# Optimization experiments

Measured on AMD Instinct MI355X. Metric: run time of the kernel, lower is better.

The kernel has to match this reference:

```python
import jax, jax.numpy as jnp
import numpy as np

U, I, NB = 200000, 100000, 50000
D = 64
NUM_LAYERS = 2
TEMP = 0.25      # conf['c_temps']
ALPHA = 0.5      # conf['alpha']
E_UI, E_UB, E_BI = 4_000_000, 2_000_000, 2_000_000
BT = 4096


def _segsum(vals, idx, gathered, n):
    # SpMM: out[idx] += vals * gathered   (COO sparse matmul)
    return jax.ops.segment_sum(vals[:, None] * gathered, idx, num_segments=n)


def _propagate(xa, xb, rows, cols, vals, layers):
    # LightGCN-style propagation over the symmetric bipartite block matrix
    # [[0, A], [A^T, 0]] with layer averaging.
    acc_a, acc_b = xa, xb
    for _ in range(layers):
        na = _segsum(vals, rows, xb[cols], xa.shape[0])
        nb = _segsum(vals, cols, xa[rows], xb.shape[0])
        xa, xb = na, nb
        acc_a = acc_a + xa
        acc_b = acc_b + xb
    inv = 1.0 / (layers + 1)
    return acc_a * inv, acc_b * inv


def _info_nce(a, b, temp):
    a = a * jax.lax.rsqrt(jnp.sum(a * a, -1, keepdims=True) + 1e-8)
    b = b * jax.lax.rsqrt(jnp.sum(b * b, -1, keepdims=True) + 1e-8)
    logits = (a @ b.T) / temp                      # [BT, BT]
    return jnp.mean(jax.nn.logsumexp(logits, axis=-1) - jnp.diagonal(logits))


def setup_inputs() -> dict:
    key = jax.random.key(0)
    ks = jax.random.split(key, 20)
    sc = 1.0 / np.sqrt(D)
    f32 = jnp.float32
    return {
        "users_feat": jax.random.normal(ks[0], (U, D), f32) * sc,
        "bundles_feat": jax.random.normal(ks[1], (NB, D), f32) * sc,
        "items_feat": jax.random.normal(ks[2], (I, D), f32) * sc,
        "L1_w": jax.random.normal(ks[3], (3, 3), f32) * 0.5,
        "L1_b": jnp.zeros((3,), f32),
        "L2_w": jax.random.normal(ks[4], (3, 3), f32) * 0.5,
        "L2_b": jnp.zeros((3,), f32),
        "L3_w": jax.random.normal(ks[5], (1, 3), f32) * 0.5,
        "L3_b": jnp.zeros((1,), f32),
        "ui_val": jax.random.uniform(ks[6], (E_UI,), f32, 0.0, 0.05),
        "ub_val": jax.random.uniform(ks[7], (E_UB,), f32, 0.0, 0.05),
        "bi_val": jax.random.uniform(ks[8], (E_BI,), f32, 0.0, 0.05),
        "ui_row": jax.random.randint(ks[9], (E_UI,), 0, U, jnp.int32),
        "ui_col": jax.random.randint(ks[10], (E_UI,), 0, I, jnp.int32),
        "ub_row": jax.random.randint(ks[11], (E_UB,), 0, U, jnp.int32),
        "ub_col": jax.random.randint(ks[12], (E_UB,), 0, NB, jnp.int32),
        "bi_row": jax.random.randint(ks[13], (E_BI,), 0, NB, jnp.int32),
        "bi_col": jax.random.randint(ks[14], (E_BI,), 0, I, jnp.int32),
        "users_idx": jax.random.randint(ks[15], (BT,), 0, U, jnp.int32),
        "bundles_idx": jax.random.randint(ks[16], (BT, 2), 0, NB, jnp.int32),
    }


def reference(users_feat, bundles_feat, items_feat, L1_w, L1_b, L2_w, L2_b,
              L3_w, L3_b, ui_val, ub_val, bi_val, ui_row, ui_col, ub_row,
              ub_col, bi_row, bi_col, users_idx, bundles_idx):
    # View 1: item-level main graph (u-i Laplacian propagation), bundle rep
    # aggregated from item embeddings via the row-normalized b-i graph.
    u1, i1 = _propagate(users_feat, items_feat, ui_row, ui_col, ui_val, NUM_LAYERS)
    b1 = _segsum(bi_val, bi_row, i1[bi_col], NB)
    # View 2: bundle-level main graph (u-b Laplacian propagation).
    u2, b2 = _propagate(users_feat, bundles_feat, ub_row, ub_col, ub_val, NUM_LAYERS)
    # View 3: sub views, one-hop row-normalized aggregation of raw item embs.
    u3 = _segsum(ui_val, ui_row, items_feat[ui_col], U)
    b3 = _segsum(bi_val, bi_row, items_feat[bi_col], NB)

    ue = jnp.stack([u1[users_idx], u2[users_idx], u3[users_idx]], axis=-1)      # [BT,D,3]
    be = jnp.stack([b1[bundles_idx], b2[bundles_idx], b3[bundles_idx]], axis=-1)  # [BT,2,D,3]
    s = jnp.einsum('bdv,bpdv->bpv', ue, be)                                      # [BT,2,3]

    # L1/L2/L3 view-fusion MLP (3 -> 3 -> 3 -> 1)
    h = jnp.tanh(s @ L1_w.T + L1_b)
    h = jnp.tanh(h @ L2_w.T + L2_b)
    pred = (h @ L3_w.T + L3_b)[..., 0]                                           # [BT,2]

    # BPR: -log sigmoid(pos - neg) == softplus(neg - pos)
    bpr = jnp.mean(jax.nn.softplus(-(pred[:, 0] - pred[:, 1])))
    cl = (_info_nce(u1[users_idx], u2[users_idx], TEMP)
          + _info_nce(b1[bundles_idx[:, 0]], b2[bundles_idx[:, 0]], TEMP))
    return bpr + ALPHA * cl
```

## Files before the change

kernel.cpp:

```cpp
#include <hip/hip_runtime.h>
#include <math.h>

#define DD 64
#define SCAN_TPB 256
#define SCAN_EPT 8
#define SCAN_EPB (SCAN_TPB * SCAN_EPT)
#define NCHUNK 8

typedef short bf16x8 __attribute__((ext_vector_type(8)));
typedef float f32x4 __attribute__((ext_vector_type(4)));

__device__ __forceinline__ float bf2f(unsigned short u) {
    return __uint_as_float(((unsigned)u) << 16);
}
__device__ __forceinline__ unsigned short f2bf(float x) {
    unsigned b = __float_as_uint(x);
    unsigned r = (b + 0x7fffu + ((b >> 16) & 1u)) >> 16;
    return (unsigned short)r;
}


__global__ void hist_chunked_kernel(int* __restrict__ cnt, const int* __restrict__ tgt,
                                    int E, int n) {
    int myc = blockIdx.x & (NCHUNK - 1);
    int sub = blockIdx.x >> 3;
    int nsub = gridDim.x >> 3;
    int start = sub * blockDim.x + threadIdx.x;
    int stride = nsub * blockDim.x;
    for (int e = start; e < E; e += stride) {
        int t_ = tgt[e];
        int c = (int)(((long long)t_ * NCHUNK) / n);
        if (c == myc) atomicAdd(&cnt[t_], 1);
    }
}

__global__ void scatter_pairs_chunked(int2* __restrict__ pairs, int* __restrict__ cursor,
                                      const int* __restrict__ tgt, const int* __restrict__ src,
                                      const float* __restrict__ val, int E, int n) {
    int myc = blockIdx.x & (NCHUNK - 1);
    int sub = blockIdx.x >> 3;
    int nsub = gridDim.x >> 3;
    int start = sub * blockDim.x + threadIdx.x;
    int stride = nsub * blockDim.x;
    for (int e = start; e < E; e += stride) {
        int t_ = tgt[e];
        int c = (int)(((long long)t_ * NCHUNK) / n);
        if (c == myc) {
            int2 pr;
            pr.x = src[e];
            pr.y = __float_as_int(val[e]);
            int p = atomicAdd(&cursor[t_], 1);
            pairs[p] = pr;
        }
    }
}

__global__ void mark_kernel(int* __restrict__ mark, const int* __restrict__ idx, int n) {
    int g = blockIdx.x * blockDim.x + threadIdx.x;
    if (g < n) mark[idx[g]] = 1;
}

__global__ void hist_marked_kernel(int* __restrict__ cnt, const int* __restrict__ tgt,
                                   const int* __restrict__ mark, int E) {
    int g = blockIdx.x * blockDim.x + threadIdx.x;
    int stride = gridDim.x * blockDim.x;
    for (int e = g; e < E; e += stride) {
        int t_ = tgt[e];
        if (mark[t_]) atomicAdd(&cnt[t_], 1);
    }
}

__global__ void scatter_marked_kernel(int2* __restrict__ pairs, int* __restrict__ cursor,
                                      const int* __restrict__ tgt, const int* __restrict__ src,
                                      const float* __restrict__ val,
                                      const int* __restrict__ mark, int E) {
    int g = blockIdx.x * blockDim.x + threadIdx.x;
    int stride = gridDim.x * blockDim.x;
    for (int e = g; e < E; e += stride) {
        int t_ = tgt[e];
        if (mark[t_]) {
            int2 pr;
            pr.x = src[e];
            pr.y = __float_as_int(val[e]);
            int p = atomicAdd(&cursor[t_], 1);
            pairs[p] = pr;
        }
    }
}

__global__ void scan_pass1(int* __restrict__ blocksum, const int* __restrict__ cnt, int n) {
    int base = blockIdx.x * SCAN_EPB + threadIdx.x * SCAN_EPT;
    int s = 0;
#pragma unroll
    for (int k = 0; k < SCAN_EPT; ++k) {
        int i = base + k;
        if (i < n) s += cnt[i];
    }
#pragma unroll
    for (int o = 32; o >= 1; o >>= 1) s += __shfl_xor(s, o);
    __shared__ int ws_[4];
    if ((threadIdx.x & 63) == 0) ws_[threadIdx.x >> 6] = s;
    __syncthreads();
    if (threadIdx.x == 0) blocksum[blockIdx.x] = ws_[0] + ws_[1] + ws_[2] + ws_[3];
}

__global__ void scan_pass2(int* __restrict__ blocksum, int nb, int* __restrict__ ptr_n) {
    __shared__ int sh[1024];
    int t = threadIdx.x;
    int v = (t < nb) ? blocksum[t] : 0;
    sh[t] = v;
    __syncthreads();
    for (int o = 1; o < 1024; o <<= 1) {
        int x = (t >= o) ? sh[t - o] : 0;
        __syncthreads();
        sh[t] += x;
        __syncthreads();
    }
    if (t < nb) blocksum[t] = sh[t] - v;
    if (t == nb - 1) ptr_n[0] = sh[t];
}

__global__ void scan_pass3(int* __restrict__ ptr, int* __restrict__ cursor,
                           const int* __restrict__ cnt, const int* __restrict__ blockoff,
                           int n) {
    int base = blockIdx.x * SCAN_EPB + threadIdx.x * SCAN_EPT;
    int vals[SCAN_EPT];
    int s = 0;
#pragma unroll
    for (int k = 0; k < SCAN_EPT; ++k) {
        int i = base + k;
        int c = (i < n) ? cnt[i] : 0;
        vals[k] = s;
        s += c;
    }
    int incl = s;
#pragma unroll
    for (int o = 1; o < 64; o <<= 1) {
        int x = __shfl_up(incl, o);
        if ((threadIdx.x & 63) >= o) incl += x;
    }
    __shared__ int wtot[4];
    if ((threadIdx.x & 63) == 63) wtot[threadIdx.x >> 6] = incl;
    __syncthreads();
    int woff = 0;
    int wv = threadIdx.x >> 6;
    for (int k = 0; k < 4; ++k)
        if (k < wv) woff += wtot[k];
    int texcl = incl - s + woff + blockoff[blockIdx.x];
#pragma unroll
    for (int k = 0; k < SCAN_EPT; ++k) {
        int i = base + k;
        if (i < n) {
            int p = texcl + vals[k];
            ptr[i] = p;
            cursor[i] = p;
        }
    }
}

__global__ void spmm2_kernel(const unsigned short* __restrict__ inb,
                             const int2* __restrict__ pairs, const int* __restrict__ ptr,
                             int nrows,
                             float* __restrict__ out, unsigned short* __restrict__ outb) {
    int wp = (int)(((unsigned)blockIdx.x * blockDim.x + threadIdx.x) >> 6);
    int lane = threadIdx.x & 63;
    int w0 = wp * 2;
    if (w0 >= nrows) return;
    bool two = (w0 + 1 < nrows);
    int pA = ptr[w0];
    int endA = ptr[w0 + 1];
    int pB = two ? endA : 0;
    int endB = two ? ptr[w0 + 2] : 0;
    float accA = 0.f, accB = 0.f;
    while (endA - pA >= 8 && endB - pB >= 8) {
        int sA[8], sB[8];
        float vA[8], vB[8];
#pragma unroll
        for (int k = 0; k < 8; ++k) {
            int2 a = pairs[pA + k];
            int2 b = pairs[pB + k];
            sA[k] = __builtin_amdgcn_readfirstlane(a.x);
            vA[k] = __int_as_float(__builtin_amdgcn_readfirstlane(a.y));
            sB[k] = __builtin_amdgcn_readfirstlane(b.x);
            vB[k] = __int_as_float(__builtin_amdgcn_readfirstlane(b.y));
        }
#pragma unroll
        for (int k = 0; k < 8; ++k) {
            accA += vA[k] * bf2f(inb[(size_t)sA[k] * DD + lane]);
            accB += vB[k] * bf2f(inb[(size_t)sB[k] * DD + lane]);
        }
        pA += 8;
        pB += 8;
    }
    for (; pA + 8 <= endA; pA += 8) {
        int ss[8];
        float vv[8];
#pragma unroll
        for (int k = 0; k < 8; ++k) {
            int2 pr = pairs[pA + k];
            ss[k] = __builtin_amdgcn_readfirstlane(pr.x);
            vv[k] = __int_as_float(__builtin_amdgcn_readfirstlane(pr.y));
        }
#pragma unroll
        for (int k = 0; k < 8; ++k) accA += vv[k] * bf2f(inb[(size_t)ss[k] * DD + lane]);
    }
    for (; pA < endA; ++pA) {
        int2 pr = pairs[pA];
        int s = __builtin_amdgcn_readfirstlane(pr.x);
        float v = __int_as_float(__builtin_amdgcn_readfirstlane(pr.y));
        accA += v * bf2f(inb[(size_t)s * DD + lane]);
    }
    for (; pB + 8 <= endB; pB += 8) {
        int ss[8];
        float vv[8];
#pragma unroll
        for (int k = 0; k < 8; ++k) {
            int2 pr = pairs[pB + k];
            ss[k] = __builtin_amdgcn_readfirstlane(pr.x);
            vv[k] = __int_as_float(__builtin_amdgcn_readfirstlane(pr.y));
        }
#pragma unroll
        for (int k = 0; k < 8; ++k) accB += vv[k] * bf2f(inb[(size_t)ss[k] * DD + lane]);
    }
    for (; pB < endB; ++pB) {
        int2 pr = pairs[pB];
        int s = __builtin_amdgcn_readfirstlane(pr.x);
        float v = __int_as_float(__builtin_amdgcn_readfirstlane(pr.y));
        accB += v * bf2f(inb[(size_t)s * DD + lane]);
    }
    size_t offA = (size_t)w0 * DD + lane;
    if (out) {
        out[offA] = accA;
        if (two) out[offA + DD] = accB;
    }
    if (outb) {
        outb[offA] = f2bf(accA);
        if (two) outb[offA + DD] = f2bf(accB);
    }
}

__global__ void spmm_kernel(const float* __restrict__ inf, const unsigned short* __restrict__ inb,
                            const int2* __restrict__ pairs, const int* __restrict__ ptr,
                            int nrows, const int* __restrict__ rowidx,
                            float* __restrict__ out, unsigned short* __restrict__ outb,
                            const float* __restrict__ add1,
                            const float* __restrict__ add2f,
                            const unsigned short* __restrict__ add2b,
                            float scale1,
                            const float* __restrict__ in2f, const unsigned short* __restrict__ in2b,
                            float* __restrict__ out2, const float* __restrict__ addB,
                            float f, float scale2,
                            unsigned short* __restrict__ nrmOut, int nrmEvery) {
    int w = (int)(((unsigned)blockIdx.x * blockDim.x + threadIdx.x) >> 6);
    int lane = threadIdx.x & 63;
    if (w >= nrows) return;
    int r = rowidx ? rowidx[w] : w;
    int p = ptr[r];
    int end = ptr[r + 1];
    size_t outoff = (size_t)w * DD + lane;
    size_t nodeoff = (size_t)r * DD + lane;
    float acc = 0.f, acc2 = 0.f;
    const bool dual = (in2f != nullptr) || (in2b != nullptr);
    for (; p + 8 <= end; p += 8) {
        int ss[8];
        float vv[8];
#pragma unroll
        for (int k = 0; k < 8; ++k) {
            int2 pr = pairs[p + k];
            ss[k] = __builtin_amdgcn_readfirstlane(pr.x);
            vv[k] = __int_as_float(__builtin_amdgcn_readfirstlane(pr.y));
        }
        if (inb) {
#pragma unroll
            for (int k = 0; k < 8; ++k) acc += vv[k] * bf2f(inb[(size_t)ss[k] * DD + lane]);
        } else {
#pragma unroll
            for (int k = 0; k < 8; ++k) acc += vv[k] * inf[(size_t)ss[k] * DD + lane];
        }
        if (dual) {
            if (in2b) {
#pragma unroll
                for (int k = 0; k < 8; ++k) acc2 += vv[k] * bf2f(in2b[(size_t)ss[k] * DD + lane]);
            } else {
#pragma unroll
                for (int k = 0; k < 8; ++k) acc2 += vv[k] * in2f[(size_t)ss[k] * DD + lane];
            }
        }
    }
    for (; p < end; ++p) {
        int2 pr = pairs[p];
        int s = __builtin_amdgcn_readfirstlane(pr.x);
        float v = __int_as_float(__builtin_amdgcn_readfirstlane(pr.y));
        acc += v * (inb ? bf2f(inb[(size_t)s * DD + lane]) : inf[(size_t)s * DD + lane]);
        if (dual)
            acc2 += v * (in2b ? bf2f(in2b[(size_t)s * DD + lane]) : in2f[(size_t)s * DD + lane]);
    }
    float rr = acc;
    if (add1) rr += add1[nodeoff];
    if (add2f) rr += add2f[nodeoff];
    if (add2b) rr += bf2f(add2b[nodeoff]);
    rr *= scale1;
    if (out) out[outoff] = rr;
    if (outb) outb[outoff] = f2bf(rr);
    if (dual) {
        float r2 = acc2 + f * acc;
        if (addB) r2 += addB[nodeoff];
        out2[outoff] = r2 * scale2;
    }
    if (nrmOut && (nrmEvery == 1 || (w & 1) == 0)) {
        float sq = rr * rr;
#pragma unroll
        for (int o = 32; o >= 1; o >>= 1) sq += __shfl_xor(sq, o);
        nrmOut[(size_t)(w / nrmEvery) * DD + lane] = f2bf(rr * rsqrtf(sq + 1e-8f));
    }
}


__global__ void f2bf_kernel(unsigned short* __restrict__ o, const float* __restrict__ i,
                            long long n4) {
    long long g = (long long)blockIdx.x * blockDim.x + threadIdx.x;
    long long stride = (long long)gridDim.x * blockDim.x;
    for (long long t = g; t < n4; t += stride) {
        float4 v = ((const float4*)i)[t];
        ushort4 u;
        u.x = f2bf(v.x); u.y = f2bf(v.y); u.z = f2bf(v.z); u.w = f2bf(v.w);
        ((ushort4*)o)[t] = u;
    }
}

__global__ void gather_rows_bf16_kernel(float* __restrict__ raw,
                                        const unsigned short* __restrict__ src,
                                        const int* __restrict__ idx, int nrows) {
    int g = blockIdx.x * blockDim.x + threadIdx.x;
    if (g >= nrows * DD) return;
    int r = g >> 6;
    raw[g] = bf2f(src[(size_t)idx[r] * DD + (g & 63)]);
}

__global__ void batch_pred_kernel(const float* __restrict__ u1b, const float* __restrict__ u2b,
                                  const float* __restrict__ u3b,
                                  const float* __restrict__ b1b, const float* __restrict__ b2b,
                                  const float* __restrict__ b3b,
                                  const float* __restrict__ W1, const float* __restrict__ c1,
                                  const float* __restrict__ W2, const float* __restrict__ c2,
                                  const float* __restrict__ W3, const float* __restrict__ c3,
                                  float* __restrict__ acc, int nb) {
    int b = blockIdx.x;
    if (b >= nb) return;
    int d = threadIdx.x;
    float ud1 = u1b[(size_t)b * DD + d];
    float ud2 = u2b[(size_t)b * DD + d];
    float ud3 = u3b[(size_t)b * DD + d];
    float pred[2];
#pragma unroll
    for (int p = 0; p < 2; ++p) {
        size_t r = (size_t)(b * 2 + p) * DD + d;
        float s0 = ud1 * b1b[r];
        float s1 = ud2 * b2b[r];
        float s2 = ud3 * b3b[r];
#pragma unroll
        for (int o = 32; o >= 1; o >>= 1) {
            s0 += __shfl_xor(s0, o);
            s1 += __shfl_xor(s1, o);
            s2 += __shfl_xor(s2, o);
        }
        float t0 = tanhf(s0 * W1[0] + s1 * W1[1] + s2 * W1[2] + c1[0]);
        float t1 = tanhf(s0 * W1[3] + s1 * W1[4] + s2 * W1[5] + c1[1]);
        float t2 = tanhf(s0 * W1[6] + s1 * W1[7] + s2 * W1[8] + c1[2]);
        float g0 = tanhf(t0 * W2[0] + t1 * W2[1] + t2 * W2[2] + c2[0]);
        float g1 = tanhf(t0 * W2[3] + t1 * W2[4] + t2 * W2[5] + c2[1]);
        float g2 = tanhf(t0 * W2[6] + t1 * W2[7] + t2 * W2[8] + c2[2]);
        pred[p] = g0 * W3[0] + g1 * W3[1] + g2 * W3[2] + c3[0];
    }
    if (d == 0) {
        float x = pred[1] - pred[0];
        float sp = (x > 20.0f) ? x : log1pf(expf(x));
        unsafeAtomicAdd(acc, sp);
    }
}

__global__ void nce_mfma_kernel(const unsigned short* __restrict__ A1,
                                const unsigned short* __restrict__ B1, float* __restrict__ acc1,
                                const unsigned short* __restrict__ A2,
                                const unsigned short* __restrict__ B2, float* __restrict__ acc2,
                                int n, float invtemp) {
    int nbv = n >> 4;
    const unsigned short* A;
    const unsigned short* B;
    float* accp;
    int blk = blockIdx.x;
    if (blk < nbv) { A = A1; B = B1; accp = acc1; }
    else           { blk -= nbv; A = A2; B = B2; accp = acc2; }
    int row0 = blk << 4;
    int wv = threadIdx.x >> 6, lane = threadIdx.x & 63;
    int li = lane & 15, lq = lane >> 4;

    const bf16x8* Ap = (const bf16x8*)(A + (size_t)(row0 + li) * DD + lq * 8);
    bf16x8 af0 = Ap[0];
    bf16x8 af1 = Ap[4];

    int qcols = n >> 2;
    int c0 = wv * qcols;
    int ntile = qcols >> 4;
    float m[4] = {-1e30f, -1e30f, -1e30f, -1e30f};
    float sm[4] = {0.f, 0.f, 0.f, 0.f};
    float dg[4] = {0.f, 0.f, 0.f, 0.f};
    for (int t = 0; t < ntile; ++t) {
        int colbase = c0 + (t << 4);
        const bf16x8* Bp = (const bf16x8*)(B + (size_t)(colbase + li) * DD + lq * 8);
        bf16x8 bf0 = Bp[0];
        bf16x8 bf1 = Bp[4];
        f32x4 z = {0.f, 0.f, 0.f, 0.f};
        f32x4 s = __builtin_amdgcn_mfma_f32_16x16x32_bf16(af0, bf0, z, 0, 0, 0);
        s = __builtin_amdgcn_mfma_f32_16x16x32_bf16(af1, bf1, s, 0, 0, 0);
        int col = colbase + li;
#pragma unroll
        for (int r = 0; r < 4; ++r) {
            float l = s[r] * invtemp;
            int row = row0 + (lq << 2) + r;
            if (col == row) dg[r] = l;
            float mn = fmaxf(m[r], l);
            sm[r] = sm[r] * __expf(m[r] - mn) + __expf(l - mn);
            m[r] = mn;
        }
    }
#pragma unroll
    for (int r = 0; r < 4; ++r) {
        float mm = m[r], ss = sm[r], dd = dg[r];
#pragma unroll
        for (int o = 1; o <= 8; o <<= 1) {
            float m2 = __shfl_xor(mm, o);
            float s2 = __shfl_xor(ss, o);
            float d2 = __shfl_xor(dd, o);
            float mn = fmaxf(mm, m2);
            ss = ss * __expf(mm - mn) + s2 * __expf(m2 - mn);
            mm = mn;
            dd += d2;
        }
        m[r] = mm; sm[r] = ss; dg[r] = dd;
    }
    __shared__ float pM[4][16], pS[4][16], pD[4][16];
    if (li == 0) {
#pragma unroll
        for (int r = 0; r < 4; ++r) {
            pM[wv][(lq << 2) + r] = m[r];
            pS[wv][(lq << 2) + r] = sm[r];
            pD[wv][(lq << 2) + r] = dg[r];
        }
    }
    __syncthreads();
    if (wv == 0 && lane < 16) {
        float mm = -1e30f, ss = 0.f, dd = 0.f;
#pragma unroll
        for (int q = 0; q < 4; ++q) {
            float mq = pM[q][lane], sq = pS[q][lane];
            dd += pD[q][lane];
            float mn = fmaxf(mm, mq);
            ss = ss * __expf(mm - mn) + sq * __expf(mq - mn);
            mm = mn;
        }
        float v = mm + logf(ss) - dd;
#pragma unroll
        for (int o = 1; o <= 8; o <<= 1) v += __shfl_xor(v, o);
        if (lane == 0) unsafeAtomicAdd(accp, v);
    }
}

__global__ void final_kernel(const float* __restrict__ acc, float* __restrict__ out,
                             float invn, float alpha) {
    out[0] = acc[0] * invn + alpha * invn * (acc[1] + acc[2]);
}


extern "C" void kernel_launch(void* const* d_in, const int* in_sizes, int n_in,
                              void* d_out, int out_size, void* d_ws, size_t ws_size,
                              hipStream_t stream) {
    const float* users_feat   = (const float*)d_in[0];
    const float* bundles_feat = (const float*)d_in[1];
    const float* items_feat   = (const float*)d_in[2];
    const float* W1 = (const float*)d_in[3];
    const float* c1 = (const float*)d_in[4];
    const float* W2 = (const float*)d_in[5];
    const float* c2 = (const float*)d_in[6];
    const float* W3 = (const float*)d_in[7];
    const float* c3 = (const float*)d_in[8];
    const float* ui_val = (const float*)d_in[9];
    const float* ub_val = (const float*)d_in[10];
    const float* bi_val = (const float*)d_in[11];
    const int* ui_row = (const int*)d_in[12];
    const int* ui_col = (const int*)d_in[13];
    const int* ub_row = (const int*)d_in[14];
    const int* ub_col = (const int*)d_in[15];
    const int* bi_row = (const int*)d_in[16];
    const int* bi_col = (const int*)d_in[17];
    const int* uidx = (const int*)d_in[18];
    const int* bidx = (const int*)d_in[19];

    const int U  = in_sizes[0] / DD;
    const int NB = in_sizes[1] / DD;
    const int I  = in_sizes[2] / DD;
    const int Eui = in_sizes[9];
    const int Eub = in_sizes[10];
    const int Ebi = in_sizes[11];
    const int BT = in_sizes[18];

    const size_t U64  = (size_t)U * DD;
    const size_t I64  = (size_t)I * DD;
    const size_t NB64 = (size_t)NB * DD;
    const size_t BT64 = (size_t)BT * DD;

    float* w = (float*)d_ws;
    size_t o = 0;
    float* RA  = w + o; o += I64;
    float* RB  = w + o; o += I64;
    float* u3b = w + o; o += BT64;
    float* u1b = w + o; o += BT64;
    float* u2b = w + o; o += BT64;
    float* b1b = w + o; o += 2 * BT64;
    float* b2b = w + o; o += 2 * BT64;
    float* b3b = w + o; o += 2 * BT64;
    unsigned short* A1  = (unsigned short*)(w + o); o += BT64 / 2;
    unsigned short* A2  = (unsigned short*)(w + o); o += BT64 / 2;
    unsigned short* B1n = (unsigned short*)(w + o); o += BT64 / 2;
    unsigned short* B2n = (unsigned short*)(w + o); o += BT64 / 2;
    float* acc = w + o; o += 16;

    unsigned short* Ubf = (unsigned short*)(w + o); o += (U64 + 1) / 2;
    unsigned short* Ibf = (unsigned short*)(w + o); o += (I64 + 1) / 2;
    unsigned short* Bbf = (unsigned short*)(w + o); o += (NB64 + 1) / 2;
    unsigned short* Xbf = (unsigned short*)(w + o); o += (U64 + 1) / 2;

    int nmax = U; if (I > nmax) nmax = I; if (NB > nmax) nmax = NB;
    int emax = Eui; if (Eub > emax) emax = Eub; if (Ebi > emax) emax = Ebi;
    int* ib = (int*)(w + o);
    size_t io_ = 0;
    int* cnt  = ib + io_; io_ += (size_t)nmax + 1;
    int* bsum = ib + io_; io_ += 1025;
    int* mark = ib + io_; io_ += (size_t)NB + 1;
    int* ptrA = ib + io_; io_ += (size_t)nmax + 1;
    int* ptrB = ib + io_; io_ += (size_t)nmax + 1;
    io_ = (io_ + 3) & ~(size_t)3;
    int2* pairsA = (int2*)(ib + io_); io_ += (size_t)emax * 2;
    int2* pairsB = (int2*)(ib + io_); io_ += (size_t)emax * 2;

    auto build = [&](int2* pairs, int* ptr_, const int* tgt, const int* src,
                     const float* val, int n, int E) {
        hipMemsetAsync(cnt, 0, ((size_t)n + 1) * sizeof(int), stream);
        hist_chunked_kernel<<<8192, 256, 0, stream>>>(cnt, tgt, E, n);
        int nb_ = (n + SCAN_EPB - 1) / SCAN_EPB;
        scan_pass1<<<nb_, SCAN_TPB, 0, stream>>>(bsum, cnt, n);
        scan_pass2<<<1, 1024, 0, stream>>>(bsum, nb_, ptr_ + n);
        scan_pass3<<<nb_, SCAN_TPB, 0, stream>>>(ptr_, cnt, cnt, bsum, n);
        scatter_pairs_chunked<<<8192, 256, 0, stream>>>(pairs, cnt, tgt, src, val, E, n);
    };
    auto spmm = [&](const float* inf, const unsigned short* inb,
                    const int2* pairs, const int* ptr_, int nrows, const int* rowidx,
                    float* out, unsigned short* outb,
                    const float* add1, const float* add2f, const unsigned short* add2b,
                    float scale1,
                    const float* in2f, const unsigned short* in2b,
                    float* out2, const float* addB, float f, float scale2,
                    unsigned short* nrmOut, int nrmEvery) {
        int blocks = (nrows + 3) / 4;
        spmm_kernel<<<blocks, 256, 0, stream>>>(inf, inb, pairs, ptr_, nrows, rowidx,
                                                out, outb, add1, add2f, add2b, scale1,
                                                in2f, in2b, out2, addB, f, scale2,
                                                nrmOut, nrmEvery);
    };
    auto spmm2 = [&](const unsigned short* inb, const int2* pairs, const int* ptr_,
                     int nrows, float* out, unsigned short* outb) {
        int blocks = (nrows + 7) / 8;
        spmm2_kernel<<<blocks, 256, 0, stream>>>(inb, pairs, ptr_, nrows, out, outb);
    };
    const float k3 = 1.0f / 3.0f;
    const float* NF = nullptr;
    const unsigned short* NB16 = nullptr;

    f2bf_kernel<<<2048, 256, 0, stream>>>(Ubf, users_feat, (long long)(U64 / 4));
    f2bf_kernel<<<1024, 256, 0, stream>>>(Ibf, items_feat, (long long)(I64 / 4));
    f2bf_kernel<<<512, 256, 0, stream>>>(Bbf, bundles_feat, (long long)(NB64 / 4));

    build(pairsA, ptrA, ui_row, ui_col, ui_val, U, Eui);
    spmm2(Ibf, pairsA, ptrA, U, nullptr, Xbf);
    gather_rows_bf16_kernel<<<(BT * DD + 255) / 256, 256, 0, stream>>>(u3b, Xbf, uidx, BT);
    build(pairsB, ptrB, ui_col, ui_row, ui_val, I, Eui);
    spmm(NF, Ubf, pairsB, ptrB, I, nullptr,
         RA, nullptr, NF, NF, NB16, 1.f,
         NF, Xbf, RB, items_feat, 1.f, k3,
         nullptr, 1);
    spmm(RA, NB16, pairsA, ptrA, BT, uidx,
         u1b, nullptr, users_feat, NF, Xbf, k3, NF, NB16, nullptr, NF, 0.f, 1.f,
         A1, 1);
    hipMemsetAsync(mark, 0, ((size_t)NB + 1) * sizeof(int), stream);
    mark_kernel<<<(2 * BT + 255) / 256, 256, 0, stream>>>(mark, bidx, 2 * BT);
    hipMemsetAsync(cnt, 0, ((size_t)NB + 1) * sizeof(int), stream);
    {
        int gb = (Ebi + 255) / 256; if (gb > 4096) gb = 4096;
        hist_marked_kernel<<<gb, 256, 0, stream>>>(cnt, bi_row, mark, Ebi);
        int nb_ = (NB + SCAN_EPB - 1) / SCAN_EPB;
        scan_pass1<<<nb_, SCAN_TPB, 0, stream>>>(bsum, cnt, NB);
        scan_pass2<<<1, 1024, 0, stream>>>(bsum, nb_, ptrA + NB);
        scan_pass3<<<nb_, SCAN_TPB, 0, stream>>>(ptrA, cnt, cnt, bsum, NB);
        scatter_marked_kernel<<<gb, 256, 0, stream>>>(pairsA, cnt, bi_row, bi_col,
                                                      bi_val, mark, Ebi);
    }
    spmm(RB, NB16, pairsA, ptrA, 2 * BT, bidx,
         b1b, nullptr, NF, NF, NB16, 1.f,
         NF, Ibf, b3b, NF, 0.f, 1.f,
         B1n, 2);

    build(pairsA, ptrA, ub_row, ub_col, ub_val, U, Eub);
    spmm2(Bbf, pairsA, ptrA, U, nullptr, Xbf);
    build(pairsB, ptrB, ub_col, ub_row, ub_val, NB, Eub);
    spmm2(Ubf, pairsB, ptrB, NB, RA, nullptr);
    spmm(RA, NB16, pairsA, ptrA, BT, uidx,
         u2b, nullptr, users_feat, NF, Xbf, k3, NF, NB16, nullptr, NF, 0.f, 1.f,
         A2, 1);
    spmm(NF, Xbf, pairsB, ptrB, 2 * BT, bidx,
         b2b, nullptr, bundles_feat, RA, NB16, k3, NF, NB16, nullptr, NF, 0.f, 1.f,
         B2n, 2);

    hipMemsetAsync(acc, 0, 4 * sizeof(float), stream);

    batch_pred_kernel<<<BT, 64, 0, stream>>>(u1b, u2b, u3b, b1b, b2b, b3b,
                                             W1, c1, W2, c2, W3, c3, acc, BT);

    nce_mfma_kernel<<<2 * (BT / 16), 256, 0, stream>>>(A1, A2, acc + 1,
                                                       B1n, B2n, acc + 2, BT, 4.0f);

    final_kernel<<<1, 1, 0, stream>>>(acc, (float*)d_out, 1.0f / (float)BT, 0.5f);
}
```

Baseline: 1.992 ms.

## Build both CSR directions in one pass and merge paired launches

```diff
diff --git a/kernel.cpp b/kernel.cpp
--- a/kernel.cpp
+++ b/kernel.cpp
@@ -18,39 +18,53 @@
     unsigned r = (b + 0x7fffu + ((b >> 16) & 1u)) >> 16;
     return (unsigned short)r;
 }
-
-
-__global__ void hist_chunked_kernel(int* __restrict__ cnt, const int* __restrict__ tgt,
-                                    int E, int n) {
+__device__ __forceinline__ int chunk_of(int t, int n) {
+    return (int)(((long long)t * NCHUNK) / n);
+}
+
+
+__global__ void hist2_chunked(int* __restrict__ cntA, const int* __restrict__ tgtA, int nA,
+                              int* __restrict__ cntB, const int* __restrict__ tgtB, int nB,
+                              int E) {
     int myc = blockIdx.x & (NCHUNK - 1);
     int sub = blockIdx.x >> 3;
     int nsub = gridDim.x >> 3;
     int start = sub * blockDim.x + threadIdx.x;
     int stride = nsub * blockDim.x;
     for (int e = start; e < E; e += stride) {
-        int t_ = tgt[e];
-        int c = (int)(((long long)t_ * NCHUNK) / n);
-        if (c == myc) atomicAdd(&cnt[t_], 1);
-    }
-}
-
-__global__ void scatter_pairs_chunked(int2* __restrict__ pairs, int* __restrict__ cursor,
-                                      const int* __restrict__ tgt, const int* __restrict__ src,
-                                      const float* __restrict__ val, int E, int n) {
+        int a = tgtA[e];
+        if (chunk_of(a, nA) == myc) atomicAdd(&cntA[a], 1);
+        int b = tgtB[e];
+        if (chunk_of(b, nB) == myc) atomicAdd(&cntB[b], 1);
+    }
+}
+
+__global__ void scatter2_chunked(int2* __restrict__ pairsA, int* __restrict__ curA, int nA,
+                                 int2* __restrict__ pairsB, int* __restrict__ curB, int nB,
+                                 const int* __restrict__ rowA, const int* __restrict__ colA,
+                                 const float* __restrict__ val, int E) {
     int myc = blockIdx.x & (NCHUNK - 1);
     int sub = blockIdx.x >> 3;
     int nsub = gridDim.x >> 3;
     int start = sub * blockDim.x + threadIdx.x;
     int stride = nsub * blockDim.x;
     for (int e = start; e < E; e += stride) {
-        int t_ = tgt[e];
-        int c = (int)(((long long)t_ * NCHUNK) / n);
-        if (c == myc) {
-            int2 pr;
-            pr.x = src[e];
-            pr.y = __float_as_int(val[e]);
-            int p = atomicAdd(&cursor[t_], 1);
-            pairs[p] = pr;
+        int r = rowA[e];
+        int ci = colA[e];
+        bool mA = (chunk_of(r, nA) == myc);
+        bool mB = (chunk_of(ci, nB) == myc);
+        if (mA || mB) {
+            int v = __float_as_int(val[e]);
+            if (mA) {
+                int p = atomicAdd(&curA[r], 1);
+                int2 pr; pr.x = ci; pr.y = v;
+                pairsA[p] = pr;
+            }
+            if (mB) {
+                int q = atomicAdd(&curB[ci], 1);
+                int2 pr; pr.x = r; pr.y = v;
+                pairsB[q] = pr;
+            }
         }
     }
 }
@@ -88,8 +102,9 @@
     }
 }
 
-__global__ void scan_pass1(int* __restrict__ blocksum, const int* __restrict__ cnt, int n) {
-    int base = blockIdx.x * SCAN_EPB + threadIdx.x * SCAN_EPT;
+__device__ __forceinline__ void scan_p1_body(int* blocksum, const int* cnt, int n, int lb,
+                                             int t) {
+    int base = lb * SCAN_EPB + t * SCAN_EPT;
     int s = 0;
 #pragma unroll
     for (int k = 0; k < SCAN_EPT; ++k) {
@@ -99,14 +114,13 @@
 #pragma unroll
     for (int o = 32; o >= 1; o >>= 1) s += __shfl_xor(s, o);
     __shared__ int ws_[4];
-    if ((threadIdx.x & 63) == 0) ws_[threadIdx.x >> 6] = s;
+    if ((t & 63) == 0) ws_[t >> 6] = s;
     __syncthreads();
-    if (threadIdx.x == 0) blocksum[blockIdx.x] = ws_[0] + ws_[1] + ws_[2] + ws_[3];
-}
-
-__global__ void scan_pass2(int* __restrict__ blocksum, int nb, int* __restrict__ ptr_n) {
+    if (t == 0) blocksum[lb] = ws_[0] + ws_[1] + ws_[2] + ws_[3];
+}
+
+__device__ __forceinline__ void scan_p2_body(int* blocksum, int nb, int* tot, int t) {
     __shared__ int sh[1024];
-    int t = threadIdx.x;
     int v = (t < nb) ? blocksum[t] : 0;
     sh[t] = v;
     __syncthreads();
@@ -117,13 +131,12 @@
         __syncthreads();
     }
     if (t < nb) blocksum[t] = sh[t] - v;
-    if (t == nb - 1) ptr_n[0] = sh[t];
-}
-
-__global__ void scan_pass3(int* __restrict__ ptr, int* __restrict__ cursor,
-                           const int* __restrict__ cnt, const int* __restrict__ blockoff,
-                           int n) {
-    int base = blockIdx.x * SCAN_EPB + threadIdx.x * SCAN_EPT;
+    if (t == nb - 1) tot[0] = sh[t];
+}
+
+__device__ __forceinline__ void scan_p3_body(int* ptr, int* cursor, const int* cnt,
+                                             const int* blockoff, int n, int lb, int t) {
+    int base = lb * SCAN_EPB + t * SCAN_EPT;
     int vals[SCAN_EPT];
     int s = 0;
 #pragma unroll
@@ -137,16 +150,16 @@
 #pragma unroll
     for (int o = 1; o < 64; o <<= 1) {
         int x = __shfl_up(incl, o);
-        if ((threadIdx.x & 63) >= o) incl += x;
+        if ((t & 63) >= o) incl += x;
     }
     __shared__ int wtot[4];
-    if ((threadIdx.x & 63) == 63) wtot[threadIdx.x >> 6] = incl;
+    if ((t & 63) == 63) wtot[t >> 6] = incl;
     __syncthreads();
     int woff = 0;
-    int wv = threadIdx.x >> 6;
+    int wv = t >> 6;
     for (int k = 0; k < 4; ++k)
         if (k < wv) woff += wtot[k];
-    int texcl = incl - s + woff + blockoff[blockIdx.x];
+    int texcl = incl - s + woff + blockoff[lb];
 #pragma unroll
     for (int k = 0; k < SCAN_EPT; ++k) {
         int i = base + k;
@@ -158,12 +171,46 @@
     }
 }
 
-__global__ void spmm2_kernel(const unsigned short* __restrict__ inb,
-                             const int2* __restrict__ pairs, const int* __restrict__ ptr,
-                             int nrows,
-                             float* __restrict__ out, unsigned short* __restrict__ outb) {
-    int wp = (int)(((unsigned)blockIdx.x * blockDim.x + threadIdx.x) >> 6);
-    int lane = threadIdx.x & 63;
+__global__ void scan_pass1(int* __restrict__ bsum, const int* __restrict__ cnt, int n) {
+    scan_p1_body(bsum, cnt, n, blockIdx.x, threadIdx.x);
+}
+__global__ void scan_pass2(int* __restrict__ bsum, int nb, int* __restrict__ tot) {
+    scan_p2_body(bsum, nb, tot, threadIdx.x);
+}
+__global__ void scan_pass3(int* __restrict__ ptr, int* __restrict__ cursor,
+                           const int* __restrict__ cnt, const int* __restrict__ boff, int n) {
+    scan_p3_body(ptr, cursor, cnt, boff, n, blockIdx.x, threadIdx.x);
+}
+
+__global__ void scan2_pass1(int* __restrict__ bsumA, const int* __restrict__ cntA, int nA,
+                            int nbA,
+                            int* __restrict__ bsumB, const int* __restrict__ cntB, int nB) {
+    int b = blockIdx.x;
+    if (b < nbA) scan_p1_body(bsumA, cntA, nA, b, threadIdx.x);
+    else         scan_p1_body(bsumB, cntB, nB, b - nbA, threadIdx.x);
+}
+__global__ void scan2_pass2(int* __restrict__ bsumA, int nbA, int* __restrict__ totA,
+                            int* __restrict__ bsumB, int nbB, int* __restrict__ totB) {
+    if (blockIdx.x == 0) scan_p2_body(bsumA, nbA, totA, threadIdx.x);
+    else                 scan_p2_body(bsumB, nbB, totB, threadIdx.x);
+}
+__global__ void scan2_pass3(int* __restrict__ ptrA, int* __restrict__ curA,
+                            const int* __restrict__ cntA, const int* __restrict__ boffA,
+                            int nA, int nbA,
+                            int* __restrict__ ptrB, int* __restrict__ curB,
+                            const int* __restrict__ cntB, const int* __restrict__ boffB,
+                            int nB) {
+    int b = blockIdx.x;
+    if (b < nbA) scan_p3_body(ptrA, curA, cntA, boffA, nA, b, threadIdx.x);
+    else         scan_p3_body(ptrB, curB, cntB, boffB, nB, b - nbA, threadIdx.x);
+}
+
+__device__ __forceinline__ void spmm2_rows(const unsigned short* __restrict__ inb,
+                                           const int2* __restrict__ pairs,
+                                           const int* __restrict__ ptr, int nrows,
+                                           float* __restrict__ out,
+                                           unsigned short* __restrict__ outb,
+                                           int wp, int lane) {
     int w0 = wp * 2;
     if (w0 >= nrows) return;
     bool two = (w0 + 1 < nrows);
@@ -207,8 +254,8 @@
     for (; pA < endA; ++pA) {
         int2 pr = pairs[pA];
         int s = __builtin_amdgcn_readfirstlane(pr.x);
-        float v = __int_as_float(__builtin_amdgcn_readfirstlane(pr.y));
-        accA += v * bf2f(inb[(size_t)s * DD + lane]);
+        accA += __int_as_float(__builtin_amdgcn_readfirstlane(pr.y)) *
+                bf2f(inb[(size_t)s * DD + lane]);
     }
     for (; pB + 8 <= endB; pB += 8) {
         int ss[8];
@@ -225,8 +272,8 @@
     for (; pB < endB; ++pB) {
         int2 pr = pairs[pB];
         int s = __builtin_amdgcn_readfirstlane(pr.x);
-        float v = __int_as_float(__builtin_amdgcn_readfirstlane(pr.y));
-        accB += v * bf2f(inb[(size_t)s * DD + lane]);
+        accB += __int_as_float(__builtin_amdgcn_readfirstlane(pr.y)) *
+                bf2f(inb[(size_t)s * DD + lane]);
     }
     size_t offA = (size_t)w0 * DD + lane;
     if (out) {
@@ -236,6 +283,32 @@
     if (outb) {
         outb[offA] = f2bf(accA);
         if (two) outb[offA + DD] = f2bf(accB);
+    }
+}
+
+__global__ void spmm2_kernel(const unsigned short* __restrict__ inb,
+                             const int2* __restrict__ pairs, const int* __restrict__ ptr,
+                             int nrows, float* __restrict__ out,
+                             unsigned short* __restrict__ outb) {
+    int wp = (int)(((unsigned)blockIdx.x * blockDim.x + threadIdx.x) >> 6);
+    spmm2_rows(inb, pairs, ptr, nrows, out, outb, wp, threadIdx.x & 63);
+}
+
+__global__ void spmm2_dual_kernel(const unsigned short* __restrict__ inbA,
+                                  const int2* __restrict__ pairsA, const int* __restrict__ ptrA,
+                                  int nrowsA, unsigned short* __restrict__ outbA,
+                                  const unsigned short* __restrict__ inbB,
+                                  const int2* __restrict__ pairsB, const int* __restrict__ ptrB,
+                                  int nrowsB, float* __restrict__ outB) {
+    int nblkA = (nrowsA + 7) / 8;
+    int blk = blockIdx.x;
+    int lane = threadIdx.x & 63;
+    int wvb = threadIdx.x >> 6;
+    if (blk < nblkA) {
+        spmm2_rows(inbA, pairsA, ptrA, nrowsA, nullptr, outbA, blk * 4 + wvb, lane);
+    } else {
+        blk -= nblkA;
+        spmm2_rows(inbB, pairsB, ptrB, nrowsB, outB, nullptr, blk * 4 + wvb, lane);
     }
 }
 
@@ -316,15 +389,26 @@
 }
 
 
-__global__ void f2bf_kernel(unsigned short* __restrict__ o, const float* __restrict__ i,
-                            long long n4) {
+__global__ void f2bf3_kernel(unsigned short* __restrict__ o1, const float* __restrict__ i1,
+                             long long n1,
+                             unsigned short* __restrict__ o2, const float* __restrict__ i2,
+                             long long n2,
+                             unsigned short* __restrict__ o3, const float* __restrict__ i3,
+                             long long n3) {
     long long g = (long long)blockIdx.x * blockDim.x + threadIdx.x;
     long long stride = (long long)gridDim.x * blockDim.x;
-    for (long long t = g; t < n4; t += stride) {
-        float4 v = ((const float4*)i)[t];
+    long long tot = n1 + n2 + n3;
+    for (long long t = g; t < tot; t += stride) {
+        const float* ip;
+        unsigned short* op;
+        long long j = t;
+        if (j < n1) { ip = i1; op = o1; }
+        else if (j < n1 + n2) { j -= n1; ip = i2; op = o2; }
+        else { j -= n1 + n2; ip = i3; op = o3; }
+        float4 v = ((const float4*)ip)[j];
         ushort4 u;
         u.x = f2bf(v.x); u.y = f2bf(v.y); u.z = f2bf(v.z); u.w = f2bf(v.w);
-        ((ushort4*)o)[t] = u;
+        ((ushort4*)op)[j] = u;
     }
 }
 
@@ -534,24 +618,31 @@
     int emax = Eui; if (Eub > emax) emax = Eub; if (Ebi > emax) emax = Ebi;
     int* ib = (int*)(w + o);
     size_t io_ = 0;
-    int* cnt  = ib + io_; io_ += (size_t)nmax + 1;
-    int* bsum = ib + io_; io_ += 1025;
-    int* mark = ib + io_; io_ += (size_t)NB + 1;
-    int* ptrA = ib + io_; io_ += (size_t)nmax + 1;
-    int* ptrB = ib + io_; io_ += (size_t)nmax + 1;
+    int* cnt   = ib + io_; io_ += (size_t)nmax + 1;
+    int* mark  = ib + io_; io_ += (size_t)NB + 1;
+    int* cnt2  = ib + io_; io_ += (size_t)nmax + 1;
+    int* bsum  = ib + io_; io_ += 1025;
+    int* bsum2 = ib + io_; io_ += 1025;
+    int* ptrA  = ib + io_; io_ += (size_t)nmax + 1;
+    int* ptrB  = ib + io_; io_ += (size_t)nmax + 1;
     io_ = (io_ + 3) & ~(size_t)3;
     int2* pairsA = (int2*)(ib + io_); io_ += (size_t)emax * 2;
     int2* pairsB = (int2*)(ib + io_); io_ += (size_t)emax * 2;
 
-    auto build = [&](int2* pairs, int* ptr_, const int* tgt, const int* src,
-                     const float* val, int n, int E) {
-        hipMemsetAsync(cnt, 0, ((size_t)n + 1) * sizeof(int), stream);
-        hist_chunked_kernel<<<8192, 256, 0, stream>>>(cnt, tgt, E, n);
-        int nb_ = (n + SCAN_EPB - 1) / SCAN_EPB;
-        scan_pass1<<<nb_, SCAN_TPB, 0, stream>>>(bsum, cnt, n);
-        scan_pass2<<<1, 1024, 0, stream>>>(bsum, nb_, ptr_ + n);
-        scan_pass3<<<nb_, SCAN_TPB, 0, stream>>>(ptr_, cnt, cnt, bsum, n);
-        scatter_pairs_chunked<<<8192, 256, 0, stream>>>(pairs, cnt, tgt, src, val, E, n);
+    const size_t zero_span = ((size_t)2 * (nmax + 1) + (NB + 1)) * sizeof(int);
+
+    auto build2 = [&](const int* rowArr, int nA, const int* colArr, int nB_, const float* val,
+                      int E) {
+        hipMemsetAsync(cnt, 0, zero_span, stream);
+        hist2_chunked<<<8192, 256, 0, stream>>>(cnt, rowArr, nA, cnt2, colArr, nB_, E);
+        int nbA = (nA + SCAN_EPB - 1) / SCAN_EPB;
+        int nbB = (nB_ + SCAN_EPB - 1) / SCAN_EPB;
+        scan2_pass1<<<nbA + nbB, SCAN_TPB, 0, stream>>>(bsum, cnt, nA, nbA, bsum2, cnt2, nB_);
+        scan2_pass2<<<2, 1024, 0, stream>>>(bsum, nbA, ptrA + nA, bsum2, nbB, ptrB + nB_);
+        scan2_pass3<<<nbA + nbB, SCAN_TPB, 0, stream>>>(ptrA, cnt, cnt, bsum, nA, nbA,
+                                                        ptrB, cnt2, cnt2, bsum2, nB_);
+        scatter2_chunked<<<8192, 256, 0, stream>>>(pairsA, cnt, nA, pairsB, cnt2, nB_,
+                                                   rowArr, colArr, val, E);
     };
     auto spmm = [&](const float* inf, const unsigned short* inb,
                     const int2* pairs, const int* ptr_, int nrows, const int* rowidx,
@@ -567,23 +658,17 @@
                                                 in2f, in2b, out2, addB, f, scale2,
                                                 nrmOut, nrmEvery);
     };
-    auto spmm2 = [&](const unsigned short* inb, const int2* pairs, const int* ptr_,
-                     int nrows, float* out, unsigned short* outb) {
-        int blocks = (nrows + 7) / 8;
-        spmm2_kernel<<<blocks, 256, 0, stream>>>(inb, pairs, ptr_, nrows, out, outb);
-    };
     const float k3 = 1.0f / 3.0f;
     const float* NF = nullptr;
     const unsigned short* NB16 = nullptr;
 
-    f2bf_kernel<<<2048, 256, 0, stream>>>(Ubf, users_feat, (long long)(U64 / 4));
-    f2bf_kernel<<<1024, 256, 0, stream>>>(Ibf, items_feat, (long long)(I64 / 4));
-    f2bf_kernel<<<512, 256, 0, stream>>>(Bbf, bundles_feat, (long long)(NB64 / 4));
-
-    build(pairsA, ptrA, ui_row, ui_col, ui_val, U, Eui);
-    spmm2(Ibf, pairsA, ptrA, U, nullptr, Xbf);
+    f2bf3_kernel<<<3072, 256, 0, stream>>>(Ubf, users_feat, (long long)(U64 / 4),
+                                           Ibf, items_feat, (long long)(I64 / 4),
+                                           Bbf, bundles_feat, (long long)(NB64 / 4));
+
+    build2(ui_row, U, ui_col, I, ui_val, Eui);
+    spmm2_kernel<<<(U + 7) / 8, 256, 0, stream>>>(Ibf, pairsA, ptrA, U, nullptr, Xbf);
     gather_rows_bf16_kernel<<<(BT * DD + 255) / 256, 256, 0, stream>>>(u3b, Xbf, uidx, BT);
-    build(pairsB, ptrB, ui_col, ui_row, ui_val, I, Eui);
     spmm(NF, Ubf, pairsB, ptrB, I, nullptr,
          RA, nullptr, NF, NF, NB16, 1.f,
          NF, Xbf, RB, items_feat, 1.f, k3,
@@ -591,9 +676,9 @@
     spmm(RA, NB16, pairsA, ptrA, BT, uidx,
          u1b, nullptr, users_feat, NF, Xbf, k3, NF, NB16, nullptr, NF, 0.f, 1.f,
          A1, 1);
-    hipMemsetAsync(mark, 0, ((size_t)NB + 1) * sizeof(int), stream);
+
+    hipMemsetAsync(cnt, 0, zero_span, stream);
     mark_kernel<<<(2 * BT + 255) / 256, 256, 0, stream>>>(mark, bidx, 2 * BT);
-    hipMemsetAsync(cnt, 0, ((size_t)NB + 1) * sizeof(int), stream);
     {
         int gb = (Ebi + 255) / 256; if (gb > 4096) gb = 4096;
         hist_marked_kernel<<<gb, 256, 0, stream>>>(cnt, bi_row, mark, Ebi);
@@ -609,10 +694,12 @@
          NF, Ibf, b3b, NF, 0.f, 1.f,
          B1n, 2);
 
-    build(pairsA, ptrA, ub_row, ub_col, ub_val, U, Eub);
-    spmm2(Bbf, pairsA, ptrA, U, nullptr, Xbf);
-    build(pairsB, ptrB, ub_col, ub_row, ub_val, NB, Eub);
-    spmm2(Ubf, pairsB, ptrB, NB, RA, nullptr);
+    build2(ub_row, U, ub_col, NB, ub_val, Eub);
+    {
+        int nblk = (U + 7) / 8 + (NB + 7) / 8;
+        spmm2_dual_kernel<<<nblk, 256, 0, stream>>>(Bbf, pairsA, ptrA, U, Xbf,
+                                                    Ubf, pairsB, ptrB, NB, RA);
+    }
     spmm(RA, NB16, pairsA, ptrA, BT, uidx,
          u2b, nullptr, users_feat, NF, Xbf, k3, NF, NB16, nullptr, NF, 0.f, 1.f,
          A2, 1);
```

Measured after the change: 1.887 ms. -5.3%, faster.
